# Kernel optimization log

Hardware: AMD Instinct MI355X
Metric: run time of the kernel (lower is better)

Reference implementation:

```python
import jax, jax.numpy as jnp
import numpy as np

N, E, F, ED, H, C, B = 50000, 200000, 768, 768, 256, 3, 4096


def setup_inputs() -> dict:
    key = jax.random.key(0)
    ks = jax.random.split(key, 20)
    s = 0.05  # init scale for params
    inp = {
        "x": jax.random.normal(ks[0], (N, F), jnp.float32),
        "edge_attr": jax.random.normal(ks[1], (E, ED), jnp.float32),
        # GATConv layer 1 (in=F, out=H, heads=1, edge_dim=ED)
        "W1": jax.random.normal(ks[2], (F, H), jnp.float32) * s,
        "as1": jax.random.normal(ks[3], (H,), jnp.float32) * s,
        "ad1": jax.random.normal(ks[4], (H,), jnp.float32) * s,
        "We1": jax.random.normal(ks[5], (ED, H), jnp.float32) * s,
        "ae1": jax.random.normal(ks[6], (H,), jnp.float32) * s,
        "b1": jnp.zeros((H,), jnp.float32),
        # GATConv layer 2 (in=H, out=H)
        "W2": jax.random.normal(ks[7], (H, H), jnp.float32) * s,
        "as2": jax.random.normal(ks[8], (H,), jnp.float32) * s,
        "ad2": jax.random.normal(ks[9], (H,), jnp.float32) * s,
        "We2": jax.random.normal(ks[10], (ED, H), jnp.float32) * s,
        "ae2": jax.random.normal(ks[11], (H,), jnp.float32) * s,
        "b2": jnp.zeros((H,), jnp.float32),
        # prediction head
        "Wp": jax.random.normal(ks[12], (H, C), jnp.float32) * s,
        "bp": jnp.zeros((C,), jnp.float32),
        "edge_index": jax.random.randint(ks[13], (2, E), 0, N, jnp.int32),
        "nodes": jax.random.randint(ks[14], (2, B), 0, N, jnp.int32),
    }
    return inp


def gat_conv(x, edge_attr, src, dst, W, a_src, a_dst, We, a_e, b, n):
    # GATConv, heads=1, edge_dim attention, add_self_loops=False
    xl = x @ W  # [n, H]
    alpha_src = (xl * a_src).sum(-1)  # [n]
    alpha_dst = (xl * a_dst).sum(-1)  # [n]
    alpha_edge = ((edge_attr @ We) * a_e).sum(-1)  # [E]
    alpha = alpha_src[src] + alpha_dst[dst] + alpha_edge  # [E]
    alpha = jax.nn.leaky_relu(alpha, 0.2)
    # scatter-softmax over incoming edges of each destination node
    m = jax.ops.segment_max(alpha, dst, num_segments=n)
    e = jnp.exp(alpha - m[dst])
    den = jax.ops.segment_sum(e, dst, num_segments=n)
    coef = e / den[dst]  # [E]
    out = jax.ops.segment_sum(coef[:, None] * xl[src], dst, num_segments=n)
    return out + b


def reference(x, edge_attr, W1, as1, ad1, We1, ae1, b1, W2, as2, ad2, We2, ae2, b2, Wp, bp, edge_index, nodes):
    src, dst = edge_index[0], edge_index[1]
    n = x.shape[0]
    h = jax.nn.relu(gat_conv(x, edge_attr, src, dst, W1, as1, ad1, We1, ae1, b1, n))
    titles = gat_conv(h, edge_attr, src, dst, W2, as2, ad2, We2, ae2, b2, n)
    c = titles[nodes[0]] * titles[nodes[1]]  # [B, H]
    return c @ Wp + bp
```

## Files before the change

kernel.cpp:

```cpp
#include <hip/hip_runtime.h>
#include <math.h>

#define HDIM 256
#define FDIM 768
#define BM 128
#define BK 32

typedef __attribute__((ext_vector_type(8))) short short8;
typedef __attribute__((ext_vector_type(4))) float f32x4;
typedef __attribute__((ext_vector_type(4))) unsigned short us4;

__device__ __forceinline__ unsigned short f2bf(float f) {
  unsigned int u = __float_as_uint(f);
  unsigned int r = (u + 0x7FFFu + ((u >> 16) & 1u)) >> 16;
  return (unsigned short)r;
}
__device__ __forceinline__ float bf2f(unsigned short b) {
  return __uint_as_float(((unsigned int)b) << 16);
}

__device__ __forceinline__ void gload_lds16(const void* g, void* l) {
  __builtin_amdgcn_global_load_lds(
      (const __attribute__((address_space(1))) void*)g,
      (__attribute__((address_space(3))) void*)l, 16, 0, 0);
}


__global__ void k_scan1(const int* __restrict__ cnt, int* __restrict__ offsets,
                        int* __restrict__ bsums, int n) {
  __shared__ int s[256];
  int i = blockIdx.x * 256 + threadIdx.x;
  int v = (i < n) ? cnt[i] : 0;
  s[threadIdx.x] = v;
  __syncthreads();
  for (int off = 1; off < 256; off <<= 1) {
    int t = (threadIdx.x >= off) ? s[threadIdx.x - off] : 0;
    __syncthreads();
    s[threadIdx.x] += t;
    __syncthreads();
  }
  if (i < n) offsets[i + 1] = s[threadIdx.x];
  if (threadIdx.x == 255) bsums[blockIdx.x] = s[255];
}

__global__ void k_scan23(int* __restrict__ offsets, int* __restrict__ cursor,
                         const int* __restrict__ bsums, int n) {
  __shared__ int s2[256];
  __shared__ int sBase;
  const int nb = (n + 255) / 256;
  const int t = threadIdx.x;
  const int bid = blockIdx.x;
  int vv = (t < nb) ? bsums[t] : 0;
  s2[t] = vv;
  __syncthreads();
  for (int off = 1; off < 256; off <<= 1) {
    int tv = (t >= off) ? s2[t - off] : 0;
    __syncthreads();
    s2[t] += tv;
    __syncthreads();
  }
  if (t == 0) sBase = (bid > 0) ? s2[bid - 1] : 0;
  __syncthreads();
  int base = sBase;
  int i = bid * 256 + t;
  if (i < n) {
    int v = offsets[i + 1] + base;
    offsets[i + 1] = v;
    if (i + 1 < n) cursor[i + 1] = v;
    if (i == 0) { offsets[0] = 0; cursor[0] = 0; }
  }
}

__global__ void k_scatter(const int* __restrict__ dst, int* __restrict__ cursor,
                          int* __restrict__ elist, int E) {
  int e = blockIdx.x * 256 + threadIdx.x;
  if (e < E) {
    int p = atomicAdd(&cursor[dst[e]], 1);
    elist[p] = e;
  }
}


__global__ __launch_bounds__(256) void k_prep(
    const float* __restrict__ We1, const float* __restrict__ ae1,
    const float* __restrict__ We2, const float* __restrict__ ae2,
    float* __restrict__ v1, float* __restrict__ v2,
    const float* __restrict__ W1, unsigned short* __restrict__ W1t,
    const float* __restrict__ W2, unsigned short* __restrict__ W2t,
    const int* __restrict__ dstArr, int* __restrict__ cnt, int E) {
  int bid = blockIdx.x;
  if (bid < 384) {
    int row = bid * 4 + (threadIdx.x >> 6);
    int lane = threadIdx.x & 63;
    const float* W = (row < FDIM) ? We1 : We2;
    const float* a = (row < FDIM) ? ae1 : ae2;
    int r = (row < FDIM) ? row : row - FDIM;
    float4 w = *(const float4*)&W[(size_t)r * HDIM + lane * 4];
    float4 av = *(const float4*)&a[lane * 4];
    float p = w.x * av.x + w.y * av.y + w.z * av.z + w.w * av.w;
    #pragma unroll
    for (int off = 32; off; off >>= 1) p += __shfl_down(p, off, 64);
    if (lane == 0) ((row < FDIM) ? v1 : v2)[r] = p;
  } else if (bid < 640) {
    int nn = bid - 384;
    for (int k = threadIdx.x; k < FDIM; k += 256)
      W1t[(size_t)nn * FDIM + k] = f2bf(W1[(size_t)k * HDIM + nn]);
  } else if (bid < 896) {
    int nn = bid - 640;
    for (int k = threadIdx.x; k < HDIM; k += 256)
      W2t[(size_t)nn * HDIM + k] = f2bf(W2[(size_t)k * HDIM + nn]);
  } else {
    int e = (bid - 896) * 256 + threadIdx.x;
    if (e < E) atomicAdd(&cnt[dstArr[e]], 1);
  }
}


template <bool AF32, bool COUTBF>
__device__ __forceinline__ void gemm_body(unsigned char* lds,
                                          const void* __restrict__ Ain,
                                          const unsigned short* __restrict__ Bt,
                                          void* __restrict__ Cout,
                                          float* __restrict__ sOut,
                                          float* __restrict__ dOut,
                                          const float* __restrict__ a_src,
                                          const float* __restrict__ a_dst,
                                          int M, int K, int tile) {
  unsigned char* As = lds;
  unsigned char* Bs = lds + 8192;
  float* partS = (float*)(lds + 24576);
  float* partD = (float*)(lds + 24576 + 2048);
  const int t = threadIdx.x;
  const int l = t & 63;
  const int w = t >> 6;
  const int wm = w >> 2, wn = w & 3;
  const int bm = tile * BM;

  f32x4 acc[4][4] = {};

  int rowA = bm + (t & 127);
  if (rowA >= M) rowA = M - 1;
  const int cA = t >> 7;
  int rowAr = bm + (t >> 2);
  if (rowAr >= M) rowAr = M - 1;
  const int kbAr = t & 3;
  const int sAr = kbAr * 2048 + (t >> 2) * 16;
  const int nB = t & 255;
  const int cB0 = t >> 8;
  const int cB1 = 2 + (t >> 8);

  int aAddr[4], bAddr[4];
  #pragma unroll
  for (int mt = 0; mt < 4; ++mt) {
    int m = wm * 64 + mt * 16 + (l & 15);
    aAddr[mt] = (l >> 4) * 2048 + m * 16;
  }
  #pragma unroll
  for (int nt = 0; nt < 4; ++nt) {
    int nn = wn * 64 + nt * 16 + (l & 15);
    bAddr[nt] = (l >> 4) * 4096 + nn * 16;
  }

  const int nsteps = K / BK;
  for (int ks = 0; ks < nsteps; ++ks) {
    const int k0 = ks * BK;
    __syncthreads();
    if (AF32) {
      const float* A = (const float*)Ain;
      const float* p = A + (size_t)rowAr * K + k0 + kbAr * 8;
      float4 f0 = *(const float4*)p;
      float4 f1 = *(const float4*)(p + 4);
      short8 hv;
      hv[0] = (short)f2bf(f0.x); hv[1] = (short)f2bf(f0.y);
      hv[2] = (short)f2bf(f0.z); hv[3] = (short)f2bf(f0.w);
      hv[4] = (short)f2bf(f1.x); hv[5] = (short)f2bf(f1.y);
      hv[6] = (short)f2bf(f1.z); hv[7] = (short)f2bf(f1.w);
      *(short8*)(As + sAr) = hv;
    } else {
      const unsigned short* A = (const unsigned short*)Ain;
      gload_lds16(A + (size_t)rowA * K + k0 + cA * 8, As + t * 16);
    }
    gload_lds16(Bt + (size_t)nB * K + k0 + cB0 * 8, Bs + t * 16);
    gload_lds16(Bt + (size_t)nB * K + k0 + cB1 * 8, Bs + 8192 + t * 16);
    __syncthreads();

    short8 af[4], bfr[4];
    #pragma unroll
    for (int mt = 0; mt < 4; ++mt) af[mt] = *(const short8*)(As + aAddr[mt]);
    #pragma unroll
    for (int nt = 0; nt < 4; ++nt) bfr[nt] = *(const short8*)(Bs + bAddr[nt]);
    #pragma unroll
    for (int mt = 0; mt < 4; ++mt)
      #pragma unroll
      for (int nt = 0; nt < 4; ++nt)
        acc[mt][nt] = __builtin_amdgcn_mfma_f32_16x16x32_bf16(af[mt], bfr[nt], acc[mt][nt], 0, 0, 0);
  }

  float asv[4], adv[4];
  #pragma unroll
  for (int nt = 0; nt < 4; ++nt) {
    int col = wn * 64 + nt * 16 + (l & 15);
    asv[nt] = a_src[col];
    adv[nt] = a_dst[col];
  }
  #pragma unroll
  for (int mt = 0; mt < 4; ++mt) {
    int rloc = wm * 64 + mt * 16 + ((l >> 4) << 2);
    #pragma unroll
    for (int r = 0; r < 4; ++r) {
      int row = bm + rloc + r;
      float ps = 0.f, pd = 0.f;
      #pragma unroll
      for (int nt = 0; nt < 4; ++nt) {
        float v = acc[mt][nt][r];
        if (row < M) {
          int col = wn * 64 + nt * 16 + (l & 15);
          if (COUTBF)
            ((unsigned short*)Cout)[(size_t)row * HDIM + col] = f2bf(v);
          else
            ((float*)Cout)[(size_t)row * HDIM + col] = v;
        }
        ps += v * asv[nt];
        pd += v * adv[nt];
      }
      #pragma unroll
      for (int off = 1; off < 16; off <<= 1) {
        ps += __shfl_xor(ps, off, 64);
        pd += __shfl_xor(pd, off, 64);
      }
      if ((l & 15) == 0) {
        partS[wn * 128 + rloc + r] = ps;
        partD[wn * 128 + rloc + r] = pd;
      }
    }
  }
  __syncthreads();
  if (t < 128) {
    int row = bm + t;
    if (row < M) {
      sOut[row] = partS[t] + partS[128 + t] + partS[256 + t] + partS[384 + t];
      dOut[row] = partD[t] + partD[128 + t] + partD[256 + t] + partD[384 + t];
    }
  }
}


__device__ __forceinline__ void edge_body(unsigned char* lds,
                                          const float* __restrict__ ea,
                                          const float* __restrict__ v1,
                                          const float* __restrict__ v2,
                                          float* __restrict__ o1,
                                          float* __restrict__ o2, int E, int ebid) {
  float* sv1 = (float*)lds;
  float* sv2 = (float*)(lds + 3072);
  for (int i = threadIdx.x; i < FDIM; i += 512) { sv1[i] = v1[i]; sv2[i] = v2[i]; }
  __syncthreads();
  int e = ebid * 8 + (threadIdx.x >> 6);
  if (e >= E) return;
  int lane = threadIdx.x & 63;
  const float* row = ea + (size_t)e * FDIM;
  float p1 = 0.f, p2 = 0.f;
  #pragma unroll
  for (int t = 0; t < 3; ++t) {
    int idx = t * 256 + lane * 4;
    float4 x = *(const float4*)&row[idx];
    float4 a = *(const float4*)&sv1[idx];
    float4 b = *(const float4*)&sv2[idx];
    p1 += x.x * a.x + x.y * a.y + x.z * a.z + x.w * a.w;
    p2 += x.x * b.x + x.y * b.y + x.z * b.z + x.w * b.w;
  }
  #pragma unroll
  for (int off = 32; off; off >>= 1) {
    p1 += __shfl_down(p1, off, 64);
    p2 += __shfl_down(p2, off, 64);
  }
  if (lane == 0) { o1[e] = p1; o2[e] = p2; }
}


__global__ __launch_bounds__(512) void k_fat1(
    const float* __restrict__ x, const unsigned short* __restrict__ W1t,
    unsigned short* __restrict__ xl1b, float* __restrict__ sArr, float* __restrict__ dArr,
    const float* __restrict__ as1, const float* __restrict__ ad1, int M,
    const float* __restrict__ ea, const float* __restrict__ v1,
    const float* __restrict__ v2, float* __restrict__ ae1Arr,
    float* __restrict__ ae2Arr, int E, int nGemm) {
  __shared__ unsigned char lds[28672];
  if ((int)blockIdx.x < nGemm)
    gemm_body<true, true>(lds, x, W1t, xl1b, sArr, dArr, as1, ad1, M, FDIM, blockIdx.x);
  else
    edge_body(lds, ea, v1, v2, ae1Arr, ae2Arr, E, blockIdx.x - nGemm);
}

__global__ __launch_bounds__(512) void k_gemm2(
    const unsigned short* __restrict__ hb, const unsigned short* __restrict__ W2t,
    unsigned short* __restrict__ xl2b, float* __restrict__ sArr, float* __restrict__ dArr,
    const float* __restrict__ as2, const float* __restrict__ ad2, int M) {
  __shared__ unsigned char lds[28672];
  gemm_body<false, true>(lds, hb, W2t, xl2b, sArr, dArr, as2, ad2, M, HDIM, blockIdx.x);
}


template <int OUTBF, int RELU>
__global__ __launch_bounds__(256) void k_aggregate(const unsigned short* __restrict__ xlb,
                                                   const float* __restrict__ sArr,
                                                   const float* __restrict__ dArr,
                                                   const float* __restrict__ aeArr,
                                                   const int* __restrict__ src,
                                                   const int* __restrict__ offsets,
                                                   const int* __restrict__ elist,
                                                   const float* __restrict__ bias,
                                                   void* __restrict__ outv, int n) {
  int node = blockIdx.x * 4 + (threadIdx.x >> 6);
  if (node >= n) return;
  int lane = threadIdx.x & 63;
  int beg = offsets[node], end = offsets[node + 1];
  float dnode = dArr[node];
  float run_m = -1e30f, run_den = 0.f;
  float a0 = 0.f, a1 = 0.f, a2 = 0.f, a3 = 0.f;
  for (int c0 = beg; c0 < end; c0 += 64) {
    int j = c0 + lane;
    float al = -1e30f;
    int sj = 0;
    if (j < end) {
      int e = elist[j];
      sj = src[e];
      float a = sArr[sj] + dnode + aeArr[e];
      al = (a > 0.f) ? a : 0.2f * a;
    }
    float cm = al;
    #pragma unroll
    for (int off = 32; off; off >>= 1) cm = fmaxf(cm, __shfl_xor(cm, off, 64));
    float new_m = fmaxf(run_m, cm);
    float ev = (j < end) ? expf(al - new_m) : 0.f;
    float csum = ev;
    #pragma unroll
    for (int off = 32; off; off >>= 1) csum += __shfl_xor(csum, off, 64);
    float scale = expf(run_m - new_m);
    run_den = run_den * scale + csum;
    a0 *= scale; a1 *= scale; a2 *= scale; a3 *= scale;
    int cdeg = end - c0;
    if (cdeg > 64) cdeg = 64;
    for (int q = 0; q < cdeg; ++q) {
      float wgt = __shfl(ev, q, 64);
      int sq = __shfl(sj, q, 64);
      us4 v = *(const us4*)(xlb + (size_t)sq * HDIM + lane * 4);
      a0 += wgt * bf2f(v[0]); a1 += wgt * bf2f(v[1]);
      a2 += wgt * bf2f(v[2]); a3 += wgt * bf2f(v[3]);
    }
    run_m = new_m;
  }
  float inv = (end > beg) ? 1.f / run_den : 0.f;
  float4 bv = *(const float4*)(bias + lane * 4);
  float o0 = a0 * inv + bv.x, o1 = a1 * inv + bv.y;
  float o2 = a2 * inv + bv.z, o3 = a3 * inv + bv.w;
  if (RELU) {
    o0 = fmaxf(o0, 0.f); o1 = fmaxf(o1, 0.f);
    o2 = fmaxf(o2, 0.f); o3 = fmaxf(o3, 0.f);
  }
  if (OUTBF) {
    us4 ov;
    ov[0] = f2bf(o0); ov[1] = f2bf(o1); ov[2] = f2bf(o2); ov[3] = f2bf(o3);
    *(us4*)((unsigned short*)outv + (size_t)node * HDIM + lane * 4) = ov;
  } else {
    *(float4*)((float*)outv + (size_t)node * HDIM + lane * 4) =
        make_float4(o0, o1, o2, o3);
  }
}


__global__ void k_head(const float* __restrict__ titles, const int* __restrict__ nodes,
                       const float* __restrict__ Wp, const float* __restrict__ bp,
                       float* __restrict__ out, int Bn) {
  int b = blockIdx.x * 4 + (threadIdx.x >> 6);
  if (b >= Bn) return;
  int lane = threadIdx.x & 63;
  const float* r0 = titles + (size_t)nodes[b] * HDIM;
  const float* r1 = titles + (size_t)nodes[Bn + b] * HDIM;
  float s0 = 0.f, s1 = 0.f, s2 = 0.f;
  #pragma unroll
  for (int i = 0; i < 4; ++i) {
    int h = lane + 64 * i;
    float c = r0[h] * r1[h];
    s0 += c * Wp[h * 3 + 0];
    s1 += c * Wp[h * 3 + 1];
    s2 += c * Wp[h * 3 + 2];
  }
  #pragma unroll
  for (int off = 32; off; off >>= 1) {
    s0 += __shfl_down(s0, off, 64);
    s1 += __shfl_down(s1, off, 64);
    s2 += __shfl_down(s2, off, 64);
  }
  if (lane == 0) {
    out[b * 3 + 0] = s0 + bp[0];
    out[b * 3 + 1] = s1 + bp[1];
    out[b * 3 + 2] = s2 + bp[2];
  }
}


extern "C" void kernel_launch(void* const* d_in, const int* in_sizes, int n_in,
                              void* d_out, int out_size, void* d_ws, size_t ws_size,
                              hipStream_t stream) {
  const float* x         = (const float*)d_in[0];
  const float* edge_attr = (const float*)d_in[1];
  const float* W1  = (const float*)d_in[2];
  const float* as1 = (const float*)d_in[3];
  const float* ad1 = (const float*)d_in[4];
  const float* We1 = (const float*)d_in[5];
  const float* ae1 = (const float*)d_in[6];
  const float* b1  = (const float*)d_in[7];
  const float* W2  = (const float*)d_in[8];
  const float* as2 = (const float*)d_in[9];
  const float* ad2 = (const float*)d_in[10];
  const float* We2 = (const float*)d_in[11];
  const float* ae2 = (const float*)d_in[12];
  const float* b2  = (const float*)d_in[13];
  const float* Wp  = (const float*)d_in[14];
  const float* bp  = (const float*)d_in[15];
  const int* edge_index = (const int*)d_in[16];
  const int* nodes      = (const int*)d_in[17];

  const int N  = in_sizes[0] / FDIM;
  const int E  = in_sizes[16] / 2;
  const int Bn = in_sizes[17] / 2;
  const int* srcArr = edge_index;
  const int* dstArr = edge_index + E;

  char* w = (char*)d_ws;
  auto carve = [&](size_t bytes) -> void* {
    void* p = (void*)w;
    w += (bytes + 255) & ~(size_t)255;
    return p;
  };
  float*          titles = (float*)carve(sizeof(float) * (size_t)N * HDIM);
  unsigned short* xl1b   = (unsigned short*)carve(2 * (size_t)N * HDIM);
  unsigned short* hb     = (unsigned short*)carve(2 * (size_t)N * HDIM);
  unsigned short* W1t    = (unsigned short*)carve(2 * (size_t)FDIM * HDIM);
  unsigned short* W2t    = (unsigned short*)carve(2 * (size_t)HDIM * HDIM);
  float* ae1Arr = (float*)carve(sizeof(float) * E);
  float* ae2Arr = (float*)carve(sizeof(float) * E);
  float* sArr = (float*)carve(sizeof(float) * N);
  float* dArr = (float*)carve(sizeof(float) * N);
  float* v1 = (float*)carve(sizeof(float) * FDIM);
  float* v2 = (float*)carve(sizeof(float) * FDIM);
  int* cnt     = (int*)carve(sizeof(int) * N);
  int* offsets = (int*)carve(sizeof(int) * (N + 1));
  int* cursor  = (int*)carve(sizeof(int) * N);
  int* elist   = (int*)carve(sizeof(int) * E);
  int* bsums   = (int*)carve(sizeof(int) * 256);

  const int nbScan = (N + 255) / 256;
  const int nbHist = (E + 255) / 256;
  const int nGemm = (N + BM - 1) / BM;
  const int nEdge = (E + 7) / 8;

  hipMemsetAsync(cnt, 0, sizeof(int) * N, stream);
  k_prep<<<896 + nbHist, 256, 0, stream>>>(We1, ae1, We2, ae2, v1, v2,
                                           W1, W1t, W2, W2t, dstArr, cnt, E);
  k_scan1<<<nbScan, 256, 0, stream>>>(cnt, offsets, bsums, N);
  k_scan23<<<nbScan, 256, 0, stream>>>(offsets, cursor, bsums, N);
  k_scatter<<<nbHist, 256, 0, stream>>>(dstArr, cursor, elist, E);

  k_fat1<<<nGemm + nEdge, 512, 0, stream>>>(x, W1t, xl1b, sArr, dArr, as1, ad1, N,
                                            edge_attr, v1, v2, ae1Arr, ae2Arr, E, nGemm);
  k_aggregate<1, 1><<<(N + 3) / 4, 256, 0, stream>>>(xl1b, sArr, dArr, ae1Arr, srcArr,
                                                     offsets, elist, b1, hb, N);
  k_gemm2<<<nGemm, 512, 0, stream>>>(hb, W2t, xl1b, sArr, dArr, as2, ad2, N);
  k_aggregate<0, 0><<<(N + 3) / 4, 256, 0, stream>>>(xl1b, sArr, dArr, ae2Arr, srcArr,
                                                     offsets, elist, b2, titles, N);
  k_head<<<(Bn + 3) / 4, 256, 0, stream>>>(titles, nodes, Wp, bp, (float*)d_out, Bn);
}
```

Baseline: 321.5 us.

## Aggregate layer-2 only for queried node pairs and fuse with prediction head

The second GAT aggregation now runs only for the 2*B nodes referenced by the prediction head, not all N nodes, and is fused with the head computation through shared memory. This avoids computing and writing the full titles tensor, which only the head reads. Each block handles two query pairs, one wave per endpoint. The result is still exact because only the gathered rows are ever used.

```diff
diff --git a/kernel.cpp b/kernel.cpp
--- a/kernel.cpp
+++ b/kernel.cpp
@@ -301,23 +301,16 @@
 }
 
 
-template <int OUTBF, int RELU>
-__global__ __launch_bounds__(256) void k_aggregate(const unsigned short* __restrict__ xlb,
-                                                   const float* __restrict__ sArr,
-                                                   const float* __restrict__ dArr,
-                                                   const float* __restrict__ aeArr,
-                                                   const int* __restrict__ src,
-                                                   const int* __restrict__ offsets,
-                                                   const int* __restrict__ elist,
-                                                   const float* __restrict__ bias,
-                                                   void* __restrict__ outv, int n) {
-  int node = blockIdx.x * 4 + (threadIdx.x >> 6);
-  if (node >= n) return;
-  int lane = threadIdx.x & 63;
-  int beg = offsets[node], end = offsets[node + 1];
-  float dnode = dArr[node];
+__device__ __forceinline__ void agg_node(const unsigned short* __restrict__ xlb,
+                                         const float* __restrict__ sArr,
+                                         float dnode,
+                                         const float* __restrict__ aeArr,
+                                         const int* __restrict__ src,
+                                         const int* __restrict__ elist,
+                                         int beg, int end, int lane,
+                                         float& a0, float& a1, float& a2, float& a3) {
   float run_m = -1e30f, run_den = 0.f;
-  float a0 = 0.f, a1 = 0.f, a2 = 0.f, a3 = 0.f;
+  a0 = a1 = a2 = a3 = 0.f;
   for (int c0 = beg; c0 < end; c0 += 64) {
     int j = c0 + lane;
     float al = -1e30f;
@@ -351,51 +344,86 @@
     run_m = new_m;
   }
   float inv = (end > beg) ? 1.f / run_den : 0.f;
+  a0 *= inv; a1 *= inv; a2 *= inv; a3 *= inv;
+}
+
+
+__global__ __launch_bounds__(256) void k_aggregate1(const unsigned short* __restrict__ xlb,
+                                                    const float* __restrict__ sArr,
+                                                    const float* __restrict__ dArr,
+                                                    const float* __restrict__ aeArr,
+                                                    const int* __restrict__ src,
+                                                    const int* __restrict__ offsets,
+                                                    const int* __restrict__ elist,
+                                                    const float* __restrict__ bias,
+                                                    unsigned short* __restrict__ outb,
+                                                    int n) {
+  int node = blockIdx.x * 4 + (threadIdx.x >> 6);
+  if (node >= n) return;
+  int lane = threadIdx.x & 63;
+  int beg = offsets[node], end = offsets[node + 1];
+  float a0, a1, a2, a3;
+  agg_node(xlb, sArr, dArr[node], aeArr, src, elist, beg, end, lane, a0, a1, a2, a3);
   float4 bv = *(const float4*)(bias + lane * 4);
-  float o0 = a0 * inv + bv.x, o1 = a1 * inv + bv.y;
-  float o2 = a2 * inv + bv.z, o3 = a3 * inv + bv.w;
-  if (RELU) {
-    o0 = fmaxf(o0, 0.f); o1 = fmaxf(o1, 0.f);
-    o2 = fmaxf(o2, 0.f); o3 = fmaxf(o3, 0.f);
-  }
-  if (OUTBF) {
-    us4 ov;
-    ov[0] = f2bf(o0); ov[1] = f2bf(o1); ov[2] = f2bf(o2); ov[3] = f2bf(o3);
-    *(us4*)((unsigned short*)outv + (size_t)node * HDIM + lane * 4) = ov;
-  } else {
-    *(float4*)((float*)outv + (size_t)node * HDIM + lane * 4) =
-        make_float4(o0, o1, o2, o3);
-  }
-}
-
-
-__global__ void k_head(const float* __restrict__ titles, const int* __restrict__ nodes,
-                       const float* __restrict__ Wp, const float* __restrict__ bp,
-                       float* __restrict__ out, int Bn) {
-  int b = blockIdx.x * 4 + (threadIdx.x >> 6);
-  if (b >= Bn) return;
+  float o0 = fmaxf(a0 + bv.x, 0.f), o1 = fmaxf(a1 + bv.y, 0.f);
+  float o2 = fmaxf(a2 + bv.z, 0.f), o3 = fmaxf(a3 + bv.w, 0.f);
+  us4 ov;
+  ov[0] = f2bf(o0); ov[1] = f2bf(o1); ov[2] = f2bf(o2); ov[3] = f2bf(o3);
+  *(us4*)(outb + (size_t)node * HDIM + lane * 4) = ov;
+}
+
+
+__global__ __launch_bounds__(256) void k_agg2head(const unsigned short* __restrict__ xl2b,
+                                                  const float* __restrict__ sArr,
+                                                  const float* __restrict__ dArr,
+                                                  const float* __restrict__ aeArr,
+                                                  const int* __restrict__ src,
+                                                  const int* __restrict__ offsets,
+                                                  const int* __restrict__ elist,
+                                                  const float* __restrict__ b2,
+                                                  const int* __restrict__ nodes,
+                                                  const float* __restrict__ Wp,
+                                                  const float* __restrict__ bp,
+                                                  float* __restrict__ out, int Bn) {
+  __shared__ float tls[2][2][HDIM];
+  int wv = threadIdx.x >> 6;
   int lane = threadIdx.x & 63;
-  const float* r0 = titles + (size_t)nodes[b] * HDIM;
-  const float* r1 = titles + (size_t)nodes[Bn + b] * HDIM;
-  float s0 = 0.f, s1 = 0.f, s2 = 0.f;
-  #pragma unroll
-  for (int i = 0; i < 4; ++i) {
-    int h = lane + 64 * i;
-    float c = r0[h] * r1[h];
-    s0 += c * Wp[h * 3 + 0];
-    s1 += c * Wp[h * 3 + 1];
-    s2 += c * Wp[h * 3 + 2];
-  }
-  #pragma unroll
-  for (int off = 32; off; off >>= 1) {
-    s0 += __shfl_down(s0, off, 64);
-    s1 += __shfl_down(s1, off, 64);
-    s2 += __shfl_down(s2, off, 64);
-  }
-  if (lane == 0) {
-    out[b * 3 + 0] = s0 + bp[0];
-    out[b * 3 + 1] = s1 + bp[1];
-    out[b * 3 + 2] = s2 + bp[2];
+  int pl = wv >> 1;
+  int side = wv & 1;
+  int b = blockIdx.x * 2 + pl;
+  if (b < Bn) {
+    int node = nodes[side * Bn + b];
+    int beg = offsets[node], end = offsets[node + 1];
+    float a0, a1, a2, a3;
+    agg_node(xl2b, sArr, dArr[node], aeArr, src, elist, beg, end, lane, a0, a1, a2, a3);
+    float4 bv = *(const float4*)(b2 + lane * 4);
+    float* dstp = &tls[pl][side][lane * 4];
+    dstp[0] = a0 + bv.x; dstp[1] = a1 + bv.y;
+    dstp[2] = a2 + bv.z; dstp[3] = a3 + bv.w;
+  }
+  __syncthreads();
+  if (b < Bn && side == 0) {
+    float4 t0 = *(const float4*)&tls[pl][0][lane * 4];
+    float4 t1 = *(const float4*)&tls[pl][1][lane * 4];
+    float c0 = t0.x * t1.x, c1 = t0.y * t1.y, c2 = t0.z * t1.z, c3 = t0.w * t1.w;
+    int h0 = lane * 4;
+    float s0 = c0 * Wp[h0 * 3 + 0] + c1 * Wp[(h0 + 1) * 3 + 0] +
+               c2 * Wp[(h0 + 2) * 3 + 0] + c3 * Wp[(h0 + 3) * 3 + 0];
+    float s1 = c0 * Wp[h0 * 3 + 1] + c1 * Wp[(h0 + 1) * 3 + 1] +
+               c2 * Wp[(h0 + 2) * 3 + 1] + c3 * Wp[(h0 + 3) * 3 + 1];
+    float s2 = c0 * Wp[h0 * 3 + 2] + c1 * Wp[(h0 + 1) * 3 + 2] +
+               c2 * Wp[(h0 + 2) * 3 + 2] + c3 * Wp[(h0 + 3) * 3 + 2];
+    #pragma unroll
+    for (int off = 32; off; off >>= 1) {
+      s0 += __shfl_down(s0, off, 64);
+      s1 += __shfl_down(s1, off, 64);
+      s2 += __shfl_down(s2, off, 64);
+    }
+    if (lane == 0) {
+      out[b * 3 + 0] = s0 + bp[0];
+      out[b * 3 + 1] = s1 + bp[1];
+      out[b * 3 + 2] = s2 + bp[2];
+    }
   }
 }
 
@@ -434,7 +462,6 @@
     w += (bytes + 255) & ~(size_t)255;
     return p;
   };
-  float*          titles = (float*)carve(sizeof(float) * (size_t)N * HDIM);
   unsigned short* xl1b   = (unsigned short*)carve(2 * (size_t)N * HDIM);
   unsigned short* hb     = (unsigned short*)carve(2 * (size_t)N * HDIM);
   unsigned short* W1t    = (unsigned short*)carve(2 * (size_t)FDIM * HDIM);
@@ -465,10 +492,10 @@
 
   k_fat1<<<nGemm + nEdge, 512, 0, stream>>>(x, W1t, xl1b, sArr, dArr, as1, ad1, N,
                                             edge_attr, v1, v2, ae1Arr, ae2Arr, E, nGemm);
-  k_aggregate<1, 1><<<(N + 3) / 4, 256, 0, stream>>>(xl1b, sArr, dArr, ae1Arr, srcArr,
-                                                     offsets, elist, b1, hb, N);
+  k_aggregate1<<<(N + 3) / 4, 256, 0, stream>>>(xl1b, sArr, dArr, ae1Arr, srcArr,
+                                                offsets, elist, b1, hb, N);
   k_gemm2<<<nGemm, 512, 0, stream>>>(hb, W2t, xl1b, sArr, dArr, as2, ad2, N);
-  k_aggregate<0, 0><<<(N + 3) / 4, 256, 0, stream>>>(xl1b, sArr, dArr, ae2Arr, srcArr,
-                                                     offsets, elist, b2, titles, N);
-  k_head<<<(Bn + 3) / 4, 256, 0, stream>>>(titles, nodes, Wp, bp, (float*)d_out, Bn);
-}
+  k_agg2head<<<(Bn + 1) / 2, 256, 0, stream>>>(xl1b, sArr, dArr, ae2Arr, srcArr,
+                                               offsets, elist, b2, nodes, Wp, bp,
+                                               (float*)d_out, Bn);
+}
```

New measurement: 289.9 us. 9.8% less time.
